# Optimization experiments

Measured on AMD Instinct MI355X. Metric: run time of the kernel, lower is better.

Reference implementation:

```python
import jax, jax.numpy as jnp
import numpy as np

NUM_FEAT = 10
C_IN = 64


def setup_inputs() -> dict:
    key = jax.random.key(0)
    ks = jax.random.split(key, 8)
    B, T, C, H, W = 1, 8, C_IN, 32, 32
    scale = 1.0 / np.sqrt(C)
    return {
        "input1": jax.random.normal(ks[0], (B, T, C, H, W), dtype=jnp.float32),
        "input2": jax.random.normal(ks[1], (B, T, C, H, W), dtype=jnp.float32),
        "w1": jax.random.normal(ks[2], (NUM_FEAT, C), dtype=jnp.float32) * scale,
        "b1": jax.random.normal(ks[3], (NUM_FEAT,), dtype=jnp.float32) * scale,
        "w2": jax.random.normal(ks[4], (NUM_FEAT, C), dtype=jnp.float32) * scale,
        "b2": jax.random.normal(ks[5], (NUM_FEAT,), dtype=jnp.float32) * scale,
        "w3": jax.random.normal(ks[6], (NUM_FEAT, C), dtype=jnp.float32) * scale,
        "b3": jax.random.normal(ks[7], (NUM_FEAT,), dtype=jnp.float32) * scale,
    }


def reference(input1, input2, w1, b1, w2, b2, w3, b3):
    B, T, C, H, W = input1.shape
    N = T * H * W
    # transpose(1,2).reshape -> [B, C, T*H*W]
    x1 = input1.transpose(0, 2, 1, 3, 4).reshape(B, C, N)
    x2 = input2.transpose(0, 2, 1, 3, 4).reshape(B, C, N)
    # 1x1 Conv1d projections (act == 0 -> ReLU branch)
    q = jnp.einsum('fc,bcn->bnf', w1, x1) + b1            # [B, N, F]
    k = jnp.einsum('fc,bcn->bfn', w2, x2) + b2[:, None]   # [B, F, N]
    v = jnp.einsum('fc,bcn->bnf', w3, x1) + b3            # [B, N, F]
    scores = jax.nn.relu(jnp.einsum('bnf,bfm->bnm', q, k))  # [B, N, N]
    out = jnp.einsum('bnm,bmf->bnf', scores, v)             # [B, N, F]
    # view([B,T,H,W,F]).permute(0,1,4,2,3)
    return out.reshape(B, T, H, W, -1).transpose(0, 1, 4, 2, 3)
```

## Files before the change

### kernel.cpp

```cpp
#include <hip/hip_runtime.h>

typedef short  s4  __attribute__((ext_vector_type(4)));
typedef float  f4  __attribute__((ext_vector_type(4)));
typedef unsigned int u2v __attribute__((ext_vector_type(2)));
typedef unsigned int uint32;
typedef unsigned short ushort16;

#define NF      10
#define CIN     64
#define NTOT    8192
#define HW      1024
#define FPAD    16
#define MSPLIT  8
#define MCHUNK  (NTOT / MSPLIT)
#define PSTRIDE 16

#if defined(__has_builtin) && __has_builtin(__builtin_amdgcn_mfma_f32_16x16x16bf16_1k)
#define MFMA16(a, b, c) __builtin_amdgcn_mfma_f32_16x16x16bf16_1k((a), (b), (c), 0, 0, 0)
#else
static __device__ inline f4 mfma16_asm(s4 a, s4 b, f4 c) {
    f4 d;
    asm volatile("s_nop 1\n\t"
                 "v_mfma_f32_16x16x16_bf16 %0, %1, %2, %3\n\t"
                 "s_nop 7\n\ts_nop 7"
                 : "=v"(d) : "v"(a), "v"(b), "v"(c));
    return d;
}
#define MFMA16(a, b, c) mfma16_asm((a), (b), (c))
#endif

static __device__ inline ushort16 f32_to_bf16_rne(float x) {
    uint32 u = __builtin_bit_cast(uint32, x);
    u = (u + 0x7fffu + ((u >> 16) & 1u)) >> 16;
    return (ushort16)u;
}

__global__ __launch_bounds__(64) void qkv_kernel(
    const float* __restrict__ in1, const float* __restrict__ in2,
    const float* __restrict__ w1, const float* __restrict__ b1,
    const float* __restrict__ w2, const float* __restrict__ b2,
    const float* __restrict__ w3, const float* __restrict__ b3,
    ushort16* __restrict__ qb, ushort16* __restrict__ kb,
    ushort16* __restrict__ vtile)
{
    const int n  = blockIdx.x * 64 + threadIdx.x;
    const int t  = n >> 10;
    const int hw = n & 1023;

    if (blockIdx.y == 0) {
        const float* p = in1 + (size_t)t * (CIN * HW) + hw;
        float aq[NF], av[NF];
#pragma unroll
        for (int f = 0; f < NF; ++f) { aq[f] = b1[f]; av[f] = b3[f]; }
#pragma unroll 8
        for (int c = 0; c < CIN; ++c) {
            float a = p[c * HW];
#pragma unroll
            for (int f = 0; f < NF; ++f) {
                aq[f] = fmaf(w1[f * CIN + c], a, aq[f]);
                av[f] = fmaf(w3[f * CIN + c], a, av[f]);
            }
        }
        ushort16 row[FPAD];
#pragma unroll
        for (int f = 0; f < NF; ++f) row[f] = f32_to_bf16_rne(aq[f]);
#pragma unroll
        for (int f = NF; f < FPAD; ++f) row[f] = 0;
        ushort16* dq = qb + (size_t)n * FPAD;
        ((uint4*)dq)[0] = ((const uint4*)row)[0];
        ((uint4*)dq)[1] = ((const uint4*)row)[1];
        const int tile = n >> 4, mi = n & 15;
        const int quad = mi >> 2, jj = mi & 3;
        ushort16* vb = vtile + (size_t)tile * 256 + jj;
#pragma unroll
        for (int f = 0; f < FPAD; ++f)
            vb[(quad * 16 + f) * 4] = (f < NF) ? f32_to_bf16_rne(av[f]) : (ushort16)0;
    } else {
        const float* p = in2 + (size_t)t * (CIN * HW) + hw;
        float ak[NF];
#pragma unroll
        for (int f = 0; f < NF; ++f) ak[f] = b2[f];
#pragma unroll 8
        for (int c = 0; c < CIN; ++c) {
            float a = p[c * HW];
#pragma unroll
            for (int f = 0; f < NF; ++f) ak[f] = fmaf(w2[f * CIN + c], a, ak[f]);
        }
        ushort16 row[FPAD];
#pragma unroll
        for (int f = 0; f < NF; ++f) row[f] = f32_to_bf16_rne(ak[f]);
#pragma unroll
        for (int f = NF; f < FPAD; ++f) row[f] = 0;
        ushort16* dk = kb + (size_t)n * FPAD;
        ((uint4*)dk)[0] = ((const uint4*)row)[0];
        ((uint4*)dk)[1] = ((const uint4*)row)[1];
    }
}

__global__ __launch_bounds__(256) void attn_mfma_kernel(
    const ushort16* __restrict__ qb, const ushort16* __restrict__ kb,
    const ushort16* __restrict__ vtile, float* __restrict__ pws)
{
    const int lane = threadIdx.x & 63;
    const int wid  = threadIdx.x >> 6;
    const int row  = lane & 15;
    const int quad = lane >> 4;
    const int n0   = blockIdx.x * 64 + wid * 16;
    const int m0   = blockIdx.y * MCHUNK;

    const s4 qf = *(const s4*)(qb + (size_t)(n0 + row) * FPAD + 4 * quad);
    const s4* kp = (const s4*)(kb + (size_t)(m0 + row) * FPAD + 4 * quad);
    const s4* vp = (const s4*)(vtile + (size_t)(m0 >> 4) * 256) + lane;

    f4 acc = {0.f, 0.f, 0.f, 0.f};
    const f4 zero = {0.f, 0.f, 0.f, 0.f};

#pragma unroll 8
    for (int s = 0; s < MCHUNK / 16; ++s) {
        s4 kf = kp[s * 64];
        s4 vf = vp[s * 64];

        f4 sc = MFMA16(kf, qf, zero);

        float r0 = fmaxf(sc[0], 0.f), r1 = fmaxf(sc[1], 0.f);
        float r2 = fmaxf(sc[2], 0.f), r3 = fmaxf(sc[3], 0.f);
        uint32 lo = __builtin_amdgcn_perm(__builtin_bit_cast(uint32, r1),
                                          __builtin_bit_cast(uint32, r0), 0x07060302u);
        uint32 hi = __builtin_amdgcn_perm(__builtin_bit_cast(uint32, r3),
                                          __builtin_bit_cast(uint32, r2), 0x07060302u);
        s4 pb = __builtin_bit_cast(s4, (u2v){lo, hi});

        acc = MFMA16(vf, pb, acc);
    }

    const int n = n0 + row;
    const int fbase = 4 * quad;
#pragma unroll
    for (int r = 0; r < 4; ++r) {
        int f = fbase + r;
        if (f < NF)
            pws[((size_t)blockIdx.y * PSTRIDE + f) * NTOT + n] = acc[r];
    }
}

__global__ __launch_bounds__(256) void reduce_kernel(
    const float* __restrict__ pws, float* __restrict__ out)
{
    const int gid = blockIdx.x * 256 + threadIdx.x;
    const int f = gid >> 13;
    const int n = gid & (NTOT - 1);
    float s = 0.f;
#pragma unroll
    for (int y = 0; y < MSPLIT; ++y)
        s += pws[((size_t)y * PSTRIDE + f) * NTOT + n];
    const int t = n >> 10, hw = n & 1023;
    out[(size_t)t * (NF * HW) + f * HW + hw] = s;
}

extern "C" void kernel_launch(void* const* d_in, const int* in_sizes, int n_in,
                              void* d_out, int out_size, void* d_ws, size_t ws_size,
                              hipStream_t stream)
{
    const float* in1 = (const float*)d_in[0];
    const float* in2 = (const float*)d_in[1];
    const float* w1  = (const float*)d_in[2];
    const float* b1  = (const float*)d_in[3];
    const float* w2  = (const float*)d_in[4];
    const float* b2  = (const float*)d_in[5];
    const float* w3  = (const float*)d_in[6];
    const float* b3  = (const float*)d_in[7];

    ushort16* qb    = (ushort16*)d_ws;
    ushort16* kb    = qb + (size_t)NTOT * FPAD;
    ushort16* vtile = kb + (size_t)NTOT * FPAD;
    float*    pws   = (float*)(vtile + (size_t)NTOT * FPAD);
    float*    out   = (float*)d_out;

    qkv_kernel<<<dim3(NTOT / 64, 2), 64, 0, stream>>>(
        in1, in2, w1, b1, w2, b2, w3, b3, qb, kb, vtile);

    attn_mfma_kernel<<<dim3(NTOT / 64, MSPLIT), 256, 0, stream>>>(qb, kb, vtile, pws);

    reduce_kernel<<<dim3(NF * NTOT / 256), 256, 0, stream>>>(pws, out);
}
```

Before: 110.2 us.

## Reuse K/V fragments across four query tiles per wave and coalesce V-tile writes

The attention kernel now has each wave handle four 16-row query groups, so each K and V fragment load feeds four MFMA pairs instead of one, which cuts global load traffic per unit of compute. The M split rises from 8 to 16 so the grid keeps enough blocks. The QKV kernel preloads all 64 input channels into registers and stages V through shared memory so the tiled layout is written with wide coalesced stores instead of scattered 2-byte stores. In exchange, register pressure rises, and the reduce step now has more partial sums to read and add.

```diff
diff --git a/kernel.cpp b/kernel.cpp
--- a/kernel.cpp
+++ b/kernel.cpp
@@ -11,7 +11,7 @@
 #define NTOT    8192
 #define HW      1024
 #define FPAD    16
-#define MSPLIT  8
+#define MSPLIT  16
 #define MCHUNK  (NTOT / MSPLIT)
 #define PSTRIDE 16
 
@@ -43,22 +43,28 @@
     ushort16* __restrict__ qb, ushort16* __restrict__ kb,
     ushort16* __restrict__ vtile)
 {
-    const int n  = blockIdx.x * 64 + threadIdx.x;
+    __shared__ ushort16 lvs[64][FPAD];
+
+    const int tid = threadIdx.x;
+    const int n  = blockIdx.x * 64 + tid;
     const int t  = n >> 10;
     const int hw = n & 1023;
 
     if (blockIdx.y == 0) {
         const float* p = in1 + (size_t)t * (CIN * HW) + hw;
+        float a[CIN];
+#pragma unroll
+        for (int c = 0; c < CIN; ++c) a[c] = p[c * HW];
+
         float aq[NF], av[NF];
 #pragma unroll
         for (int f = 0; f < NF; ++f) { aq[f] = b1[f]; av[f] = b3[f]; }
-#pragma unroll 8
+#pragma unroll
         for (int c = 0; c < CIN; ++c) {
-            float a = p[c * HW];
 #pragma unroll
             for (int f = 0; f < NF; ++f) {
-                aq[f] = fmaf(w1[f * CIN + c], a, aq[f]);
-                av[f] = fmaf(w3[f * CIN + c], a, av[f]);
+                aq[f] = fmaf(w1[f * CIN + c], a[c], aq[f]);
+                av[f] = fmaf(w3[f * CIN + c], a[c], av[f]);
             }
         }
         ushort16 row[FPAD];
@@ -69,22 +75,37 @@
         ushort16* dq = qb + (size_t)n * FPAD;
         ((uint4*)dq)[0] = ((const uint4*)row)[0];
         ((uint4*)dq)[1] = ((const uint4*)row)[1];
-        const int tile = n >> 4, mi = n & 15;
-        const int quad = mi >> 2, jj = mi & 3;
-        ushort16* vb = vtile + (size_t)tile * 256 + jj;
-#pragma unroll
-        for (int f = 0; f < FPAD; ++f)
-            vb[(quad * 16 + f) * 4] = (f < NF) ? f32_to_bf16_rne(av[f]) : (ushort16)0;
+
+#pragma unroll
+        for (int f = 0; f < NF; ++f) lvs[tid][f] = f32_to_bf16_rne(av[f]);
+#pragma unroll
+        for (int f = NF; f < FPAD; ++f) lvs[tid][f] = 0;
+        __syncthreads();
+        const int quad = (tid & 15) >> 2;
+        const int tloc = tid >> 4;
+        ushort16 obuf[16];
+#pragma unroll
+        for (int e = 0; e < 16; ++e) {
+            int f  = ((tid & 3) * 4 + (e >> 2)) & 15;
+            int mi = quad * 4 + (e & 3);
+            obuf[e] = lvs[tloc * 16 + mi][f];
+        }
+        ushort16* dv = vtile + (size_t)blockIdx.x * 1024 + tid * 16;
+        ((uint4*)dv)[0] = ((const uint4*)obuf)[0];
+        ((uint4*)dv)[1] = ((const uint4*)obuf)[1];
     } else {
         const float* p = in2 + (size_t)t * (CIN * HW) + hw;
+        float a[CIN];
+#pragma unroll
+        for (int c = 0; c < CIN; ++c) a[c] = p[c * HW];
+
         float ak[NF];
 #pragma unroll
         for (int f = 0; f < NF; ++f) ak[f] = b2[f];
-#pragma unroll 8
+#pragma unroll
         for (int c = 0; c < CIN; ++c) {
-            float a = p[c * HW];
-#pragma unroll
-            for (int f = 0; f < NF; ++f) ak[f] = fmaf(w2[f * CIN + c], a, ak[f]);
+#pragma unroll
+            for (int f = 0; f < NF; ++f) ak[f] = fmaf(w2[f * CIN + c], a[c], ak[f]);
         }
         ushort16 row[FPAD];
 #pragma unroll
@@ -105,41 +126,50 @@
     const int wid  = threadIdx.x >> 6;
     const int row  = lane & 15;
     const int quad = lane >> 4;
-    const int n0   = blockIdx.x * 64 + wid * 16;
+    const int nb   = blockIdx.x * 256 + wid * 64;
     const int m0   = blockIdx.y * MCHUNK;
 
-    const s4 qf = *(const s4*)(qb + (size_t)(n0 + row) * FPAD + 4 * quad);
+    s4 qf[4];
+#pragma unroll
+    for (int g = 0; g < 4; ++g)
+        qf[g] = *(const s4*)(qb + (size_t)(nb + g * 16 + row) * FPAD + 4 * quad);
+
     const s4* kp = (const s4*)(kb + (size_t)(m0 + row) * FPAD + 4 * quad);
     const s4* vp = (const s4*)(vtile + (size_t)(m0 >> 4) * 256) + lane;
 
-    f4 acc = {0.f, 0.f, 0.f, 0.f};
+    f4 acc[4];
+#pragma unroll
+    for (int g = 0; g < 4; ++g) acc[g] = (f4){0.f, 0.f, 0.f, 0.f};
     const f4 zero = {0.f, 0.f, 0.f, 0.f};
 
-#pragma unroll 8
+#pragma unroll 4
     for (int s = 0; s < MCHUNK / 16; ++s) {
         s4 kf = kp[s * 64];
         s4 vf = vp[s * 64];
-
-        f4 sc = MFMA16(kf, qf, zero);
-
-        float r0 = fmaxf(sc[0], 0.f), r1 = fmaxf(sc[1], 0.f);
-        float r2 = fmaxf(sc[2], 0.f), r3 = fmaxf(sc[3], 0.f);
-        uint32 lo = __builtin_amdgcn_perm(__builtin_bit_cast(uint32, r1),
-                                          __builtin_bit_cast(uint32, r0), 0x07060302u);
-        uint32 hi = __builtin_amdgcn_perm(__builtin_bit_cast(uint32, r3),
-                                          __builtin_bit_cast(uint32, r2), 0x07060302u);
-        s4 pb = __builtin_bit_cast(s4, (u2v){lo, hi});
-
-        acc = MFMA16(vf, pb, acc);
+#pragma unroll
+        for (int g = 0; g < 4; ++g) {
+            f4 sc = MFMA16(kf, qf[g], zero);
+            float r0 = fmaxf(sc[0], 0.f), r1 = fmaxf(sc[1], 0.f);
+            float r2 = fmaxf(sc[2], 0.f), r3 = fmaxf(sc[3], 0.f);
+            uint32 lo = __builtin_amdgcn_perm(__builtin_bit_cast(uint32, r1),
+                                              __builtin_bit_cast(uint32, r0), 0x07060302u);
+            uint32 hi = __builtin_amdgcn_perm(__builtin_bit_cast(uint32, r3),
+                                              __builtin_bit_cast(uint32, r2), 0x07060302u);
+            s4 pb = __builtin_bit_cast(s4, (u2v){lo, hi});
+            acc[g] = MFMA16(vf, pb, acc[g]);
+        }
     }
 
-    const int n = n0 + row;
     const int fbase = 4 * quad;
 #pragma unroll
-    for (int r = 0; r < 4; ++r) {
-        int f = fbase + r;
-        if (f < NF)
-            pws[((size_t)blockIdx.y * PSTRIDE + f) * NTOT + n] = acc[r];
+    for (int g = 0; g < 4; ++g) {
+        const int n = nb + g * 16 + row;
+#pragma unroll
+        for (int r = 0; r < 4; ++r) {
+            int f = fbase + r;
+            if (f < NF)
+                pws[((size_t)blockIdx.y * PSTRIDE + f) * NTOT + n] = acc[g][r];
+        }
     }
 }
 
@@ -179,7 +209,7 @@
     qkv_kernel<<<dim3(NTOT / 64, 2), 64, 0, stream>>>(
         in1, in2, w1, b1, w2, b2, w3, b3, qb, kb, vtile);
 
-    attn_mfma_kernel<<<dim3(NTOT / 64, MSPLIT), 256, 0, stream>>>(qb, kb, vtile, pws);
+    attn_mfma_kernel<<<dim3(NTOT / 256, MSPLIT), 256, 0, stream>>>(qb, kb, vtile, pws);
 
     reduce_kernel<<<dim3(NF * NTOT / 256), 256, 0, stream>>>(pws, out);
 }
```

New measurement: 106.3 us. 1.04x faster.
